# Optimization experiments

Hardware: AMD Instinct MI355X
Metric: run time of the kernel (lower is better)

## Reference

```python
import jax, jax.numpy as jnp
import numpy as np


def conv1d(x, w, b, pad):
    # x: [N, Cin, L], w: [Cout, Cin, K] (torch OIH layout)
    out = jax.lax.conv_general_dilated(
        x, w, window_strides=(1,), padding=[(pad, pad)],
        dimension_numbers=("NCH", "OIH", "NCH"))
    return out + b[None, :, None]


def adaptive_avg_pool1d(x, out_size):
    # Faithful torch AdaptiveAvgPool1d: bin i covers [floor(i*L/D), ceil((i+1)*L/D))
    L = x.shape[-1]
    i = jnp.arange(out_size)
    starts = (i * L) // out_size
    ends = ((i + 1) * L + out_size - 1) // out_size
    zeros = jnp.zeros(x.shape[:-1] + (1,), dtype=x.dtype)
    cs = jnp.concatenate([zeros, jnp.cumsum(x, axis=-1)], axis=-1)
    counts = (ends - starts).astype(x.dtype)
    return (cs[..., ends] - cs[..., starts]) / counts


def setup_inputs() -> dict:
    key = jax.random.key(0)
    ks = jax.random.split(key, 12)
    B, C, T, D = 16, 64, 1024, 1024  # output_dim must equal seq_len (broadcast in forward)
    s = lambda fan: 1.0 / np.sqrt(fan)
    return {
        "eeg_data": jax.random.normal(ks[0], (B, C, T), jnp.float32),
        "filter_strength": jnp.ones((1,), jnp.float32),
        # spectral_attention params
        "aw1": jax.random.normal(ks[1], (32, 1, 64), jnp.float32) * s(64),
        "ab1": jnp.zeros((32,), jnp.float32),
        "aw2": jax.random.normal(ks[2], (64, 32, 32), jnp.float32) * s(32 * 32),
        "ab2": jnp.zeros((64,), jnp.float32),
        "aw3": jax.random.normal(ks[3], (1, 64, 1), jnp.float32) * s(64),
        "ab3": jnp.zeros((1,), jnp.float32),
        # feature_projection params
        "fw1": jax.random.normal(ks[4], (64, 1, 128), jnp.float32) * s(128),
        "fb1": jnp.zeros((64,), jnp.float32),
        "bn_g": jnp.ones((64,), jnp.float32),
        "bn_b": jnp.zeros((64,), jnp.float32),
        "bn_m": jnp.zeros((64,), jnp.float32),
        "bn_v": jnp.ones((64,), jnp.float32),
        "fw2": jax.random.normal(ks[5], (D, 64, 1), jnp.float32) * s(64),
        "fb2": jnp.zeros((D,), jnp.float32),
    }


def reference(eeg_data, filter_strength, aw1, ab1, aw2, ab2, aw3, ab3,
              fw1, fb1, bn_g, bn_b, bn_m, bn_v, fw2, fb2):
    B, C, T = eeg_data.shape
    D = fw2.shape[0]
    EPS = 1e-5
    # LearnableBandpassFilter: elementwise scale
    filt = eeg_data * filter_strength
    # spectral attention over channel-averaged signal
    ca = jnp.mean(filt, axis=1, keepdims=True)           # [B,1,T]
    a = jax.nn.relu(conv1d(ca, aw1, ab1, 32))            # [B,32,T+1]
    a = jax.nn.relu(conv1d(a, aw2, ab2, 16))             # [B,64,T+2]
    a = adaptive_avg_pool1d(a, D)                        # [B,64,D]
    attn = jax.nn.sigmoid(conv1d(a, aw3, ab3, 0))        # [B,1,D], D==T
    attended = filt * attn                               # [B,C,T]
    # feature_projection: shared weights over channels -> batch the python loop
    x = attended.reshape(B * C, 1, T)
    h = conv1d(x, fw1, fb1, 64)                          # [B*C,64,T+1]
    h = (h - bn_m[None, :, None]) * jax.lax.rsqrt(bn_v[None, :, None] + EPS)
    h = h * bn_g[None, :, None] + bn_b[None, :, None]
    h = jax.nn.relu(h)
    h = adaptive_avg_pool1d(h, D)                        # [B*C,64,D]
    h = conv1d(h, fw2, fb2, 0)                           # [B*C,D,D]
    feats = h.reshape(B, C, D, D).mean(axis=1)           # mean over channels
    return feats, attn[:, 0, :]
```

## Files before the change

### kernel.cpp

```cpp
#include <hip/hip_runtime.h>
#include <math.h>

#define Bn 16
#define Cn 64
#define Tn 1024
#define Dn 1024

#define CA_S   1088
#define CA_OFF 0
#define AT_OFF 17408
#define SA_OFF 33792
#define A1_S   1072
#define A1_OFF 50176
#define A2_S   1026
#define A2_OFF 599040
#define XS_U   (2*50176)
#define HS_S   1040
#define HS_OFF 2671616
#define HB_OFF 4801536

#define A1S_U  (2*HS_OFF)
#define HBT_U  (2*HB_OFF)
#define WFW2_U (HBT_U + 1048576)
#define WAW2_U (WFW2_U + 65536)
#define WFW1_U (WAW2_U + 65536)

typedef __attribute__((ext_vector_type(4))) float f32x4;
typedef __attribute__((ext_vector_type(8))) short bf16x8;
typedef __attribute__((ext_vector_type(4))) unsigned int u32x4;

static __device__ inline unsigned short f2bf(float x) {
  unsigned u = __builtin_bit_cast(unsigned, x);
  return (unsigned short)((u + 0x7fffu + ((u >> 16) & 1u)) >> 16);
}

__global__ void k0_zero(const float* __restrict__ aw2, const float* __restrict__ fw2,
                        const float* __restrict__ fw1, float* __restrict__ ws) {
  int id = blockIdx.x * 256 + threadIdx.x;
  if (id < 17408) {
    ws[CA_OFF + id] = 0.f;
  } else if (id < 33792) {
    ws[SA_OFF + (id - 17408)] = 0.f;
  } else if (id < 57856) {
    int id2 = id - 33792;
    int row = id2 / 47, j = id2 % 47;
    int pos = (j < 16) ? j : (1041 + j - 16);
    ws[A1_OFF + row * A1_S + pos] = 0.f;
  } else if (id < 74240) {
    int e0 = (id - 57856) * 4;
    float4 f = *(const float4*)&aw2[e0];
    unsigned short* d = (unsigned short*)ws + WAW2_U + e0;
    d[0] = f2bf(f.x); d[1] = f2bf(f.y); d[2] = f2bf(f.z); d[3] = f2bf(f.w);
  } else if (id < 90624) {
    int e0 = (id - 74240) * 4;
    float4 f = *(const float4*)&fw2[e0];
    unsigned short* d = (unsigned short*)ws + WFW2_U + e0;
    d[0] = f2bf(f.x); d[1] = f2bf(f.y); d[2] = f2bf(f.z); d[3] = f2bf(f.w);
  } else if (id < 92672) {
    int e0 = (id - 90624) * 4;
    float4 f = *(const float4*)&fw1[e0];
    unsigned short* d = (unsigned short*)ws + WFW1_U + e0;
    d[0] = f2bf(f.x); d[1] = f2bf(f.y); d[2] = f2bf(f.z); d[3] = f2bf(f.w);
  }
}

__global__ void k1_ca(const float* __restrict__ eeg, const float* __restrict__ fsp,
                      float* __restrict__ ws) {
  int b = blockIdx.y, t = blockIdx.x * 256 + threadIdx.x;
  int c0 = blockIdx.z * 8;
  float s = 0.f;
#pragma unroll
  for (int j = 0; j < 8; ++j) s += eeg[(b * 64 + c0 + j) * 1024 + t];
  atomicAdd(&ws[CA_OFF + b * CA_S + 32 + t], s * fsp[0] * (1.f / 64.f));
}

__global__ void k2_conv1(const float* __restrict__ aw1, const float* __restrict__ ab1,
                         float* __restrict__ ws) {
  int t = blockIdx.x * 256 + threadIdx.x;
  int o = blockIdx.y, b = blockIdx.z;
  if (t >= 1025) return;
  const float* cab = ws + CA_OFF + b * CA_S;
  float acc = ab1[o];
#pragma unroll 8
  for (int k = 0; k < 64; ++k) acc += aw1[o * 64 + k] * cab[t + k];
  ws[A1_OFF + (b * 32 + o) * A1_S + 16 + t] = fmaxf(acc, 0.f);
}

__global__ void k2b_a1s(float* __restrict__ ws) {
  int row = blockIdx.x;
  int tid = threadIdx.x;
  __shared__ unsigned short xl[1232];
  const float* src = ws + A1_OFF + row * A1_S;
  for (int i = tid; i < 1232; i += 256) {
    float v = (i < 1072) ? src[i] : 0.f;
    xl[i] = f2bf(v);
  }
  __syncthreads();
  unsigned short* a1s = (unsigned short*)ws + A1S_U;
  for (int q = tid; q < 608; q += 256) {
    int s = q / 152, mm = q % 152;
    int e = mm * 8;
    unsigned a0 = xl[e + s + 0], a1 = xl[e + s + 1], a2 = xl[e + s + 2], a3 = xl[e + s + 3];
    unsigned a4 = xl[e + s + 4], a5 = xl[e + s + 5], a6 = xl[e + s + 6], a7 = xl[e + s + 7];
    uint4 v;
    v.x = a0 | (a1 << 16); v.y = a2 | (a3 << 16); v.z = a4 | (a5 << 16); v.w = a6 | (a7 << 16);
    *(uint4*)&a1s[(s * 512 + row) * 1216 + e] = v;
  }
}

__global__ __launch_bounds__(256) void k3_mfma(const float* __restrict__ ab2,
                                               float* __restrict__ ws) {
  int t0 = blockIdx.x * 64, b = blockIdx.y, oh = blockIdx.z;
  int tid = threadIdx.x, l = tid & 63, w = tid >> 6;
  __shared__ unsigned short wlds[16 * 1032];
  __shared__ unsigned short xlds[32 * 4 * 104];
  const unsigned short* wb = (const unsigned short*)ws + WAW2_U;
  const unsigned short* a1s = (const unsigned short*)ws + A1S_U;
#pragma unroll
  for (int r = 0; r < 8; ++r) {
    int idx = tid + r * 256;
    int o = idx >> 7, j = idx & 127;
    *(uint4*)&wlds[o * 1032 + j * 8] = *(const uint4*)&wb[(oh * 16 + o) * 1024 + j * 8];
  }
#pragma unroll
  for (int r = 0; r < 6; ++r) {
    int idx = tid + r * 256;
    int i = idx / 48, rem = idx % 48, s = rem / 12, mm = rem % 12;
    *(uint4*)&xlds[(i * 4 + s) * 104 + mm * 8] =
        *(const uint4*)&a1s[(s * 512 + b * 32 + i) * 1216 + t0 + mm * 8];
  }
  __syncthreads();
  int m = l & 15, q = l >> 4;
  int A0 = w * 16 + m + q * 8;
  int xoffb = (A0 & 3) * 104 + (A0 & ~3);
  f32x4 acc = (f32x4){0.f, 0.f, 0.f, 0.f};
  for (int i = 0; i < 32; ++i) {
    const uint2* p = (const uint2*)&xlds[i * 416 + xoffb];
    uint2 lo = p[0], hi = p[1];
    u32x4 bb; bb.x = lo.x; bb.y = lo.y; bb.z = hi.x; bb.w = hi.y;
    u32x4 a = *(const u32x4*)&wlds[m * 1032 + i * 32 + q * 8];
    acc = __builtin_amdgcn_mfma_f32_16x16x32_bf16(
        __builtin_bit_cast(bf16x8, a), __builtin_bit_cast(bf16x8, bb), acc, 0, 0, 0);
  }
  int t = t0 + w * 16 + m;
  if (t < 1026) {
#pragma unroll
    for (int r = 0; r < 4; ++r) {
      int o = oh * 16 + q * 4 + r;
      ws[A2_OFF + (b * 64 + o) * A2_S + t] = fmaxf(acc[r] + ab2[o], 0.f);
    }
  }
}

__global__ void k4a_part(const float* __restrict__ aw3, float* __restrict__ ws) {
  int b = blockIdx.y, t = blockIdx.x * 256 + threadIdx.x;
  int i0 = blockIdx.z * 16;
  int s = t + (t >= 512 ? 1 : 0);
  float acc = 0.f;
#pragma unroll
  for (int ii = 0; ii < 16; ++ii) {
    const float* row = ws + A2_OFF + (b * 64 + i0 + ii) * A2_S;
    acc += aw3[i0 + ii] * 0.5f * (row[s] + row[s + 1]);
  }
  atomicAdd(&ws[SA_OFF + b * 1024 + t], acc);
}

__global__ void k4c_sig(const float* __restrict__ ab3, float* __restrict__ ws,
                        float* __restrict__ out) {
  int b = blockIdx.y, t = blockIdx.x * 256 + threadIdx.x;
  float a = 1.f / (1.f + expf(-(ws[SA_OFF + b * 1024 + t] + ab3[0])));
  ws[AT_OFF + b * 1024 + t] = a;
  out[16777216 + b * 1024 + t] = a;
}

__global__ void k4b_xs(const float* __restrict__ eeg, const float* __restrict__ fsp,
                       float* __restrict__ ws) {
  int bc = blockIdx.x;
  int b = bc >> 6;
  int tid = threadIdx.x;
  __shared__ unsigned short xsl[1288];
  float fs = fsp[0];
  for (int i = tid; i < 1288; i += 256) {
    int j = i - 64;
    float v = 0.f;
    if (j >= 0 && j < 1024) v = eeg[bc * 1024 + j] * fs * ws[AT_OFF + b * 1024 + j];
    xsl[i] = f2bf(v);
  }
  __syncthreads();
  unsigned short* xsg = (unsigned short*)ws + XS_U;
  for (int q = tid; q < 640; q += 256) {
    int s = q / 160, m = q % 160, e = m * 8;
    uint4 v;
    unsigned a0 = xsl[e + s + 0], a1 = xsl[e + s + 1], a2 = xsl[e + s + 2], a3 = xsl[e + s + 3];
    unsigned a4 = xsl[e + s + 4], a5 = xsl[e + s + 5], a6 = xsl[e + s + 6], a7 = xsl[e + s + 7];
    v.x = a0 | (a1 << 16); v.y = a2 | (a3 << 16); v.z = a4 | (a5 << 16); v.w = a6 | (a7 << 16);
    *(uint4*)&xsg[(s * 1024 + bc) * 1280 + e] = v;
  }
}

__global__ __launch_bounds__(256, 2) void k5_mfma(
    const float* __restrict__ fb1,
    const float* __restrict__ bng, const float* __restrict__ bnb,
    const float* __restrict__ bnm, const float* __restrict__ bnv,
    float* __restrict__ ws) {
  int t0 = blockIdx.x * 64, b = blockIdx.y, g2 = blockIdx.z;
  int tid = threadIdx.x, l = tid & 63, w = tid >> 6;
  __shared__ unsigned short wlds[64 * 128];
  __shared__ unsigned short xlds[32 * 4 * 200];
  const unsigned short* wbf = (const unsigned short*)ws + WFW1_U;
#pragma unroll
  for (int r = 0; r < 4; ++r) {
    int idx = tid + r * 256;
    *(uint4*)&wlds[idx * 8] = *(const uint4*)&wbf[idx * 8];
  }
  const unsigned short* xsg = (const unsigned short*)ws + XS_U;
#pragma unroll
  for (int r = 0; r < 12; ++r) {
    int q = tid + r * 256;
    int ch = q / 96, rem = q % 96, s = rem / 24, m = rem % 24;
    int c = g2 * 32 + ch;
    uint4 v = *(const uint4*)&xsg[((s * 1024) + b * 64 + c) * 1280 + t0 + m * 8];
    *(uint4*)&xlds[(ch * 4 + s) * 200 + m * 8] = v;
  }
  int row0 = (l >> 4) * 4;
  float scv[4][4], shv[4][4];
#pragma unroll
  for (int mt = 0; mt < 4; ++mt)
#pragma unroll
    for (int r = 0; r < 4; ++r) {
      int o = mt * 16 + row0 + r;
      float s = bng[o] * rsqrtf(bnv[o] + 1e-5f);
      scv[mt][r] = s;
      shv[mt][r] = (fb1[o] - bnm[o]) * s + bnb[o];
    }
  __syncthreads();
  u32x4 wf[4][4];
#pragma unroll
  for (int mt = 0; mt < 4; ++mt)
#pragma unroll
    for (int ks = 0; ks < 4; ++ks)
      wf[mt][ks] = *(const u32x4*)&wlds[(mt * 16 + (l & 15)) * 128 + ks * 32 + (l >> 4) * 8];
  int xoff[4];
#pragma unroll
  for (int ks = 0; ks < 4; ++ks) {
    int A0 = (l & 15) + ks * 32 + (l >> 4) * 8;
    int s = A0 & 3, e = A0 & ~3;
    xoff[ks] = s * 200 + w * 16 + e;
  }
  f32x4 acc[4];
#pragma unroll
  for (int mt = 0; mt < 4; ++mt) acc[mt] = (f32x4){0.f, 0.f, 0.f, 0.f};
  for (int ch = 0; ch < 32; ++ch) {
    u32x4 bf[4];
#pragma unroll
    for (int ks = 0; ks < 4; ++ks) {
      const uint2* p = (const uint2*)&xlds[ch * 800 + xoff[ks]];
      uint2 lo = p[0], hi = p[1];
      u32x4 bb; bb.x = lo.x; bb.y = lo.y; bb.z = hi.x; bb.w = hi.y;
      bf[ks] = bb;
    }
#pragma unroll
    for (int mt = 0; mt < 4; ++mt) {
      f32x4 c = (f32x4){0.f, 0.f, 0.f, 0.f};
#pragma unroll
      for (int ks = 0; ks < 4; ++ks)
        c = __builtin_amdgcn_mfma_f32_16x16x32_bf16(
            __builtin_bit_cast(bf16x8, wf[mt][ks]),
            __builtin_bit_cast(bf16x8, bf[ks]), c, 0, 0, 0);
#pragma unroll
      for (int r = 0; r < 4; ++r)
        acc[mt][r] += fmaxf(c[r] * scv[mt][r] + shv[mt][r], 0.f);
    }
  }
  int t = t0 + w * 16 + (l & 15);
  if (t < 1025) {
#pragma unroll
    for (int mt = 0; mt < 4; ++mt)
#pragma unroll
      for (int r = 0; r < 4; ++r)
        ws[HS_OFF + (((g2 * 16 + b) * 64) + mt * 16 + row0 + r) * HS_S + t] = acc[mt][r];
  }
}

__global__ void k5b_t(float* __restrict__ ws) {
  int tt = blockIdx.x, b = blockIdx.y;
  int tid = threadIdx.x;
  __shared__ unsigned short tr[64 * 80];
  int k = tid >> 2, q = tid & 3;
  const float* r0 = ws + HS_OFF + ((0 + b) * 64 + k) * HS_S + tt * 64;
  const float* r1 = ws + HS_OFF + ((16 + b) * 64 + k) * HS_S + tt * 64;
#pragma unroll
  for (int j = 0; j < 16; ++j) {
    int tl = q * 16 + j;
    float v = r0[tl] + r0[tl + 1] + r1[tl] + r1[tl + 1];
    tr[tl * 80 + k] = f2bf(v * (1.f / 128.f));
  }
  __syncthreads();
  unsigned short* hbT = (unsigned short*)ws + HBT_U;
#pragma unroll
  for (int r = 0; r < 2; ++r) {
    int idx = tid + r * 256;
    int tl = idx >> 3, j = idx & 7;
    uint4 v = *(uint4*)&tr[tl * 80 + j * 8];
    *(uint4*)&hbT[(b * 1024 + tt * 64 + tl) * 64 + j * 8] = v;
  }
}

__global__ __launch_bounds__(256) void k6_mfma(const float* __restrict__ fb2,
                                               float* __restrict__ ws,
                                               float* __restrict__ out) {
  int tt = blockIdx.x, dt = blockIdx.y, b = blockIdx.z;
  int tid = threadIdx.x, l = tid & 63, w = tid >> 6;
  int wd = w >> 1, wt = w & 1;
  __shared__ unsigned short wA[64 * 80], xB[64 * 80];
  const unsigned short* w2 = (const unsigned short*)ws + WFW2_U;
  const unsigned short* hbT = (const unsigned short*)ws + HBT_U;
#pragma unroll
  for (int r = 0; r < 2; ++r) {
    int idx = tid + r * 256;
    int row = idx >> 3, j = idx & 7;
    *(uint4*)&wA[row * 80 + j * 8] = *(const uint4*)&w2[(dt * 64 + row) * 64 + j * 8];
    *(uint4*)&xB[row * 80 + j * 8] = *(const uint4*)&hbT[(b * 1024 + tt * 64 + row) * 64 + j * 8];
  }
  __syncthreads();
  int m = l & 15, q = l >> 4;
  f32x4 acc[2][2];
#pragma unroll
  for (int mt = 0; mt < 2; ++mt)
#pragma unroll
    for (int nt = 0; nt < 2; ++nt) acc[mt][nt] = (f32x4){0.f, 0.f, 0.f, 0.f};
#pragma unroll
  for (int ks = 0; ks < 2; ++ks) {
    u32x4 a[2], bb[2];
#pragma unroll
    for (int mt = 0; mt < 2; ++mt)
      a[mt] = *(const u32x4*)&wA[(wd * 32 + mt * 16 + m) * 80 + ks * 32 + q * 8];
#pragma unroll
    for (int nt = 0; nt < 2; ++nt)
      bb[nt] = *(const u32x4*)&xB[(wt * 32 + nt * 16 + m) * 80 + ks * 32 + q * 8];
#pragma unroll
    for (int mt = 0; mt < 2; ++mt)
#pragma unroll
      for (int nt = 0; nt < 2; ++nt)
        acc[mt][nt] = __builtin_amdgcn_mfma_f32_16x16x32_bf16(
            __builtin_bit_cast(bf16x8, a[mt]), __builtin_bit_cast(bf16x8, bb[nt]),
            acc[mt][nt], 0, 0, 0);
  }
#pragma unroll
  for (int mt = 0; mt < 2; ++mt) {
#pragma unroll
    for (int r = 0; r < 4; ++r) {
      int d = dt * 64 + wd * 32 + mt * 16 + q * 4 + r;
      float bias = fb2[d];
#pragma unroll
      for (int nt = 0; nt < 2; ++nt) {
        int t = tt * 64 + wt * 32 + nt * 16 + m;
        out[(b * 1024 + d) * 1024 + t] = acc[mt][nt][r] + bias;
      }
    }
  }
}

extern "C" void kernel_launch(void* const* d_in, const int* in_sizes, int n_in,
                              void* d_out, int out_size, void* d_ws, size_t ws_size,
                              hipStream_t stream) {
  const float* eeg = (const float*)d_in[0];
  const float* fsp = (const float*)d_in[1];
  const float* aw1 = (const float*)d_in[2];
  const float* ab1 = (const float*)d_in[3];
  const float* aw2 = (const float*)d_in[4];
  const float* ab2 = (const float*)d_in[5];
  const float* aw3 = (const float*)d_in[6];
  const float* ab3 = (const float*)d_in[7];
  const float* fw1 = (const float*)d_in[8];
  const float* fb1 = (const float*)d_in[9];
  const float* bng = (const float*)d_in[10];
  const float* bnb = (const float*)d_in[11];
  const float* bnm = (const float*)d_in[12];
  const float* bnv = (const float*)d_in[13];
  const float* fw2 = (const float*)d_in[14];
  const float* fb2 = (const float*)d_in[15];
  float* out = (float*)d_out;
  float* ws = (float*)d_ws;

  hipLaunchKernelGGL(k0_zero, dim3(362), dim3(256), 0, stream, aw2, fw2, fw1, ws);
  hipLaunchKernelGGL(k1_ca, dim3(4, 16, 8), dim3(256), 0, stream, eeg, fsp, ws);
  hipLaunchKernelGGL(k2_conv1, dim3(5, 32, 16), dim3(256), 0, stream, aw1, ab1, ws);
  hipLaunchKernelGGL(k2b_a1s, dim3(512), dim3(256), 0, stream, ws);
  hipLaunchKernelGGL(k3_mfma, dim3(17, 16, 4), dim3(256), 0, stream, ab2, ws);
  hipLaunchKernelGGL(k4a_part, dim3(4, 16, 4), dim3(256), 0, stream, aw3, ws);
  hipLaunchKernelGGL(k4c_sig, dim3(4, 16), dim3(256), 0, stream, ab3, ws, out);
  hipLaunchKernelGGL(k4b_xs, dim3(1024), dim3(256), 0, stream, eeg, fsp, ws);
  hipLaunchKernelGGL(k5_mfma, dim3(17, 16, 2), dim3(256), 0, stream,
                     fb1, bng, bnb, bnm, bnv, ws);
  hipLaunchKernelGGL(k5b_t, dim3(16, 16), dim3(256), 0, stream, ws);
  hipLaunchKernelGGL(k6_mfma, dim3(16, 16, 16), dim3(256), 0, stream, fb2, ws, out);
}
```

Measured before the change: 185.6 us.

## Fuse small attention-path kernels and drop atomics and weight LDS staging

Merges the zeroing and channel-mean kernels into one init kernel that sums all 64 channels per thread and writes directly, with no atomics and no pre-zeroing. Fuses conv1 into the bf16 shift-pack kernel through shared memory, so the fp32 intermediate buffer is no longer needed. Fuses the partial attention reduction with the sigmoid into one kernel. In k5, weights are loaded straight from global memory into registers instead of staging through LDS, and the occupancy hint is raised to 3. The intent is fewer launches, less global traffic and fewer atomics, at the cost of less parallelism in the fused reductions (for example only 64 blocks for the channel mean).

```diff
diff --git a/kernel.cpp b/kernel.cpp
--- a/kernel.cpp
+++ b/kernel.cpp
@@ -9,9 +9,6 @@
 #define CA_S   1088
 #define CA_OFF 0
 #define AT_OFF 17408
-#define SA_OFF 33792
-#define A1_S   1072
-#define A1_OFF 50176
 #define A2_S   1026
 #define A2_OFF 599040
 #define XS_U   (2*50176)
@@ -34,66 +31,55 @@
   return (unsigned short)((u + 0x7fffu + ((u >> 16) & 1u)) >> 16);
 }
 
-__global__ void k0_zero(const float* __restrict__ aw2, const float* __restrict__ fw2,
+__global__ void kI_init(const float* __restrict__ eeg, const float* __restrict__ fsp,
+                        const float* __restrict__ aw2, const float* __restrict__ fw2,
                         const float* __restrict__ fw1, float* __restrict__ ws) {
-  int id = blockIdx.x * 256 + threadIdx.x;
-  if (id < 17408) {
-    ws[CA_OFF + id] = 0.f;
-  } else if (id < 33792) {
-    ws[SA_OFF + (id - 17408)] = 0.f;
-  } else if (id < 57856) {
-    int id2 = id - 33792;
-    int row = id2 / 47, j = id2 % 47;
-    int pos = (j < 16) ? j : (1041 + j - 16);
-    ws[A1_OFF + row * A1_S + pos] = 0.f;
-  } else if (id < 74240) {
-    int e0 = (id - 57856) * 4;
+  int bx = blockIdx.x, tid = threadIdx.x;
+  if (bx < 64) {
+    int b = bx >> 2, x = bx & 3;
+    int t = x * 256 + tid;
+    float s = 0.f;
+#pragma unroll 8
+    for (int c = 0; c < 64; ++c) s += eeg[(b * 64 + c) * 1024 + t];
+    ws[CA_OFF + b * CA_S + 32 + t] = s * fsp[0] * (1.f / 64.f);
+    if (x == 0 && tid < 32) ws[CA_OFF + b * CA_S + tid] = 0.f;
+    if (x == 3 && tid >= 224) ws[CA_OFF + b * CA_S + 1056 + (tid - 224)] = 0.f;
+    return;
+  }
+  int id = (bx - 64) * 256 + tid;
+  if (id < 16384) {
+    int e0 = id * 4;
     float4 f = *(const float4*)&aw2[e0];
     unsigned short* d = (unsigned short*)ws + WAW2_U + e0;
     d[0] = f2bf(f.x); d[1] = f2bf(f.y); d[2] = f2bf(f.z); d[3] = f2bf(f.w);
-  } else if (id < 90624) {
-    int e0 = (id - 74240) * 4;
+  } else if (id < 32768) {
+    int e0 = (id - 16384) * 4;
     float4 f = *(const float4*)&fw2[e0];
     unsigned short* d = (unsigned short*)ws + WFW2_U + e0;
     d[0] = f2bf(f.x); d[1] = f2bf(f.y); d[2] = f2bf(f.z); d[3] = f2bf(f.w);
-  } else if (id < 92672) {
-    int e0 = (id - 90624) * 4;
+  } else if (id < 34816) {
+    int e0 = (id - 32768) * 4;
     float4 f = *(const float4*)&fw1[e0];
     unsigned short* d = (unsigned short*)ws + WFW1_U + e0;
     d[0] = f2bf(f.x); d[1] = f2bf(f.y); d[2] = f2bf(f.z); d[3] = f2bf(f.w);
   }
 }
 
-__global__ void k1_ca(const float* __restrict__ eeg, const float* __restrict__ fsp,
-                      float* __restrict__ ws) {
-  int b = blockIdx.y, t = blockIdx.x * 256 + threadIdx.x;
-  int c0 = blockIdx.z * 8;
-  float s = 0.f;
-#pragma unroll
-  for (int j = 0; j < 8; ++j) s += eeg[(b * 64 + c0 + j) * 1024 + t];
-  atomicAdd(&ws[CA_OFF + b * CA_S + 32 + t], s * fsp[0] * (1.f / 64.f));
-}
-
-__global__ void k2_conv1(const float* __restrict__ aw1, const float* __restrict__ ab1,
-                         float* __restrict__ ws) {
-  int t = blockIdx.x * 256 + threadIdx.x;
-  int o = blockIdx.y, b = blockIdx.z;
-  if (t >= 1025) return;
-  const float* cab = ws + CA_OFF + b * CA_S;
-  float acc = ab1[o];
-#pragma unroll 8
-  for (int k = 0; k < 64; ++k) acc += aw1[o * 64 + k] * cab[t + k];
-  ws[A1_OFF + (b * 32 + o) * A1_S + 16 + t] = fmaxf(acc, 0.f);
-}
-
-__global__ void k2b_a1s(float* __restrict__ ws) {
+__global__ void k2s_conv1(const float* __restrict__ aw1, const float* __restrict__ ab1,
+                          float* __restrict__ ws) {
   int row = blockIdx.x;
+  int b = row >> 5, o = row & 31;
   int tid = threadIdx.x;
   __shared__ unsigned short xl[1232];
-  const float* src = ws + A1_OFF + row * A1_S;
-  for (int i = tid; i < 1232; i += 256) {
-    float v = (i < 1072) ? src[i] : 0.f;
-    xl[i] = f2bf(v);
+  for (int i = tid; i < 1232; i += 256)
+    if (i < 16 || i >= 1041) xl[i] = 0;
+  const float* cab = ws + CA_OFF + b * CA_S;
+  float bias = ab1[o];
+  for (int t = tid; t < 1025; t += 256) {
+    float acc = bias;
+#pragma unroll 8
+    for (int k = 0; k < 64; ++k) acc += aw1[o * 64 + k] * cab[t + k];
+    xl[16 + t] = f2bf(fmaxf(acc, 0.f));
   }
   __syncthreads();
   unsigned short* a1s = (unsigned short*)ws + A1S_U;
@@ -152,23 +138,17 @@
   }
 }
 
-__global__ void k4a_part(const float* __restrict__ aw3, float* __restrict__ ws) {
+__global__ void k4_attn(const float* __restrict__ aw3, const float* __restrict__ ab3,
+                        float* __restrict__ ws, float* __restrict__ out) {
   int b = blockIdx.y, t = blockIdx.x * 256 + threadIdx.x;
-  int i0 = blockIdx.z * 16;
   int s = t + (t >= 512 ? 1 : 0);
   float acc = 0.f;
-#pragma unroll
-  for (int ii = 0; ii < 16; ++ii) {
-    const float* row = ws + A2_OFF + (b * 64 + i0 + ii) * A2_S;
-    acc += aw3[i0 + ii] * 0.5f * (row[s] + row[s + 1]);
-  }
-  atomicAdd(&ws[SA_OFF + b * 1024 + t], acc);
-}
-
-__global__ void k4c_sig(const float* __restrict__ ab3, float* __restrict__ ws,
-                        float* __restrict__ out) {
-  int b = blockIdx.y, t = blockIdx.x * 256 + threadIdx.x;
-  float a = 1.f / (1.f + expf(-(ws[SA_OFF + b * 1024 + t] + ab3[0])));
+#pragma unroll 8
+  for (int i = 0; i < 64; ++i) {
+    const float* row = ws + A2_OFF + (b * 64 + i) * A2_S;
+    acc += aw3[i] * (row[s] + row[s + 1]);
+  }
+  float a = 1.f / (1.f + expf(-(acc * 0.5f + ab3[0])));
   ws[AT_OFF + b * 1024 + t] = a;
   out[16777216 + b * 1024 + t] = a;
 }
@@ -198,21 +178,15 @@
   }
 }
 
-__global__ __launch_bounds__(256, 2) void k5_mfma(
+__global__ __launch_bounds__(256, 3) void k5_mfma(
     const float* __restrict__ fb1,
     const float* __restrict__ bng, const float* __restrict__ bnb,
     const float* __restrict__ bnm, const float* __restrict__ bnv,
     float* __restrict__ ws) {
   int t0 = blockIdx.x * 64, b = blockIdx.y, g2 = blockIdx.z;
   int tid = threadIdx.x, l = tid & 63, w = tid >> 6;
-  __shared__ unsigned short wlds[64 * 128];
   __shared__ unsigned short xlds[32 * 4 * 200];
   const unsigned short* wbf = (const unsigned short*)ws + WFW1_U;
-#pragma unroll
-  for (int r = 0; r < 4; ++r) {
-    int idx = tid + r * 256;
-    *(uint4*)&wlds[idx * 8] = *(const uint4*)&wbf[idx * 8];
-  }
   const unsigned short* xsg = (const unsigned short*)ws + XS_U;
 #pragma unroll
   for (int r = 0; r < 12; ++r) {
@@ -222,6 +196,12 @@
     uint4 v = *(const uint4*)&xsg[((s * 1024) + b * 64 + c) * 1280 + t0 + m * 8];
     *(uint4*)&xlds[(ch * 4 + s) * 200 + m * 8] = v;
   }
+  u32x4 wf[4][4];
+#pragma unroll
+  for (int mt = 0; mt < 4; ++mt)
+#pragma unroll
+    for (int ks = 0; ks < 4; ++ks)
+      wf[mt][ks] = *(const u32x4*)&wbf[(mt * 16 + (l & 15)) * 128 + ks * 32 + (l >> 4) * 8];
   int row0 = (l >> 4) * 4;
   float scv[4][4], shv[4][4];
 #pragma unroll
@@ -233,13 +213,6 @@
       scv[mt][r] = s;
       shv[mt][r] = (fb1[o] - bnm[o]) * s + bnb[o];
     }
-  __syncthreads();
-  u32x4 wf[4][4];
-#pragma unroll
-  for (int mt = 0; mt < 4; ++mt)
-#pragma unroll
-    for (int ks = 0; ks < 4; ++ks)
-      wf[mt][ks] = *(const u32x4*)&wlds[(mt * 16 + (l & 15)) * 128 + ks * 32 + (l >> 4) * 8];
   int xoff[4];
 #pragma unroll
   for (int ks = 0; ks < 4; ++ks) {
@@ -247,6 +220,7 @@
     int s = A0 & 3, e = A0 & ~3;
     xoff[ks] = s * 200 + w * 16 + e;
   }
+  __syncthreads();
   f32x4 acc[4];
 #pragma unroll
   for (int mt = 0; mt < 4; ++mt) acc[mt] = (f32x4){0.f, 0.f, 0.f, 0.f};
@@ -383,13 +357,10 @@
   float* out = (float*)d_out;
   float* ws = (float*)d_ws;
 
-  hipLaunchKernelGGL(k0_zero, dim3(362), dim3(256), 0, stream, aw2, fw2, fw1, ws);
-  hipLaunchKernelGGL(k1_ca, dim3(4, 16, 8), dim3(256), 0, stream, eeg, fsp, ws);
-  hipLaunchKernelGGL(k2_conv1, dim3(5, 32, 16), dim3(256), 0, stream, aw1, ab1, ws);
-  hipLaunchKernelGGL(k2b_a1s, dim3(512), dim3(256), 0, stream, ws);
+  hipLaunchKernelGGL(kI_init, dim3(200), dim3(256), 0, stream, eeg, fsp, aw2, fw2, fw1, ws);
+  hipLaunchKernelGGL(k2s_conv1, dim3(512), dim3(256), 0, stream, aw1, ab1, ws);
   hipLaunchKernelGGL(k3_mfma, dim3(17, 16, 4), dim3(256), 0, stream, ab2, ws);
-  hipLaunchKernelGGL(k4a_part, dim3(4, 16, 4), dim3(256), 0, stream, aw3, ws);
-  hipLaunchKernelGGL(k4c_sig, dim3(4, 16), dim3(256), 0, stream, ab3, ws, out);
+  hipLaunchKernelGGL(k4_attn, dim3(4, 16), dim3(256), 0, stream, aw3, ab3, ws, out);
   hipLaunchKernelGGL(k4b_xs, dim3(1024), dim3(256), 0, stream, eeg, fsp, ws);
   hipLaunchKernelGGL(k5_mfma, dim3(17, 16, 2), dim3(256), 0, stream,
                      fb1, bng, bnb, bnm, bnv, ws);
```

Result: faster. 178.3 us (-3.9%).
